# Optimization experiments

Measured on AMD Instinct MI355X. Metric: run time of the kernel, lower is better.

The kernel has to match this reference:

```python
import jax, jax.numpy as jnp
import numpy as np

IN_DIM = 512
OUT_DIM = 512
GRID_SIZE = 7
K = 4
N_KNOTS = GRID_SIZE + 2 * K + 1  # 16
N_BASIS = GRID_SIZE + K          # 11
BATCH = 16384


def b_splines(x, grid, k):
    # x: (B, in_dim), grid: (in_dim, N_KNOTS)
    x = x[..., None]  # (B, in, 1)
    value = ((x >= grid[:, :-1]) & (x < grid[:, 1:])).astype(x.dtype)  # (B, in, N_KNOTS-1)
    for p in range(1, k + 1):
        diff_left = grid[:, p:-1] - grid[:, :-(p + 1)]
        diff_right = grid[:, p + 1:] - grid[:, 1:-p]
        safe_dl = jnp.where(diff_left != 0, diff_left, 1.0)
        safe_dr = jnp.where(diff_right != 0, diff_right, 1.0)
        ratio_left = jnp.where(diff_left != 0, (x - grid[:, :-(p + 1)]) / safe_dl, 0.0)
        ratio_right = jnp.where(diff_right != 0, (grid[:, p + 1:] - x) / safe_dr, 0.0)
        value = (ratio_left * value[..., :-1] + ratio_right * value[..., 1:]) / (
            ratio_left + ratio_right + 1e-8)
    return value  # (B, in, N_BASIS)


def setup_inputs() -> dict:
    key = jax.random.key(0)
    k1, k2, k3, k4 = jax.random.split(key, 4)
    x = jax.random.uniform(k1, (BATCH, IN_DIM), dtype=jnp.float32)
    grid = jnp.tile(jnp.linspace(-1.0, 1.0, N_KNOTS, dtype=jnp.float32)[None, :], (IN_DIM, 1))
    coeff = jax.random.normal(k2, (OUT_DIM, IN_DIM, N_BASIS), dtype=jnp.float32) * 0.05
    scale_base = 1.0 / IN_DIM ** 0.5 + (
        jax.random.normal(k3, (OUT_DIM, IN_DIM), dtype=jnp.float32) * 2.0 - 1.0) * 0.05
    scale_spline = jnp.ones((OUT_DIM, IN_DIM), dtype=jnp.float32)
    bias = jnp.zeros((1, OUT_DIM), dtype=jnp.float32)
    return {"x": x, "grid": grid, "coeff": coeff, "scale_base": scale_base,
            "scale_spline": scale_spline, "bias": bias}


def reference(x, grid, coeff, scale_base, scale_spline, bias):
    shape = x.shape[:-1]
    x2 = x.reshape(-1, IN_DIM)
    splines = b_splines(x2, grid, K)                         # (B, in, N_BASIS)
    base_act = x2 + jnp.sin(x2)                              # KolmogorovActivation
    y_b = jnp.einsum('bi,oi->bo', base_act, scale_base)
    y_spline = jnp.einsum('bik,oik->bo', splines, coeff * scale_spline[:, :, None])
    y = y_b + y_spline + bias
    return y.reshape(*shape, OUT_DIM)
```

## Files before the change

kernel.cpp:

```cpp
#include <hip/hip_runtime.h>
#include <hip/hip_bf16.h>
#include <stdint.h>

#define IN_DIM  512
#define OUT_DIM 512
#define BATCH   16384
#define BM      128
#define BN      256
#define BK      96
#define KCH     64
#define TSTR    104
#define TILE_U  3072
#define TILE_EL 24576

typedef __bf16 bf16;
typedef __bf16 bf16x8 __attribute__((ext_vector_type(8)));
typedef float  f32x4  __attribute__((ext_vector_type(4)));

__device__ __forceinline__ uint bfbits(float v) {
    union { bf16 h; ushort u; } c; c.h = (bf16)v; return (uint)c.u;
}
__device__ __forceinline__ uint pk2(float lo, float hi) {
    return bfbits(lo) | (bfbits(hi) << 16);
}

__global__ void pack_w(const float* __restrict__ coeff,
                       const float* __restrict__ sbase,
                       const float* __restrict__ sspl,
                       bf16* __restrict__ W3) {
    __shared__ __align__(16) bf16 L[256 * 96];
    const int t  = threadIdx.x;
    const int g  = blockIdx.x >> 6;
    const int kc = blockIdx.x & 63;
    const int o  = g * 256 + t;
    const float* cp = coeff + ((size_t)o * 512 + kc * 8) * 11;
    const float* sp = sspl  + (size_t)o * 512 + kc * 8;
    const float* bp = sbase + (size_t)o * 512 + kc * 8;
    union { bf16 h[96]; uint4 q[12]; } rw;
#pragma unroll
    for (int il = 0; il < 8; ++il) {
        const float s = sp[il];
#pragma unroll
        for (int k = 0; k < 11; ++k) rw.h[il * 12 + k] = (bf16)(cp[il * 11 + k] * s);
        rw.h[il * 12 + 11] = (bf16)bp[il];
    }
    uint4* lrow = (uint4*)(L + t * 96);
#pragma unroll
    for (int j = 0; j < 12; ++j) lrow[j] = rw.q[j];
    __syncthreads();
    uint4* dst = (uint4*)W3 + (size_t)(g * 64 + kc) * TILE_U;
#pragma unroll
    for (int uu = 0; uu < 12; ++uu) {
        const int U   = uu * 256 + t;
        const int rb  = U / 192;
        const int rem = U - rb * 192;
        const int s   = rem >> 6;
        const int li  = rem & 63;
        const int lq  = li >> 4, lr = li & 15;
        dst[U] = *(const uint4*)(L + (rb * 16 + lr) * 96 + s * 32 + lq * 8);
    }
}


#define LOAD_B(Barr, kcn)                                                     \
  {                                                                           \
    const bf16* _bb = WgB + (size_t)(kcn) * TILE_EL + boff;                   \
    _Pragma("unroll")                                                         \
    for (int f = 0; f < 12; ++f)                                              \
      Barr[f] = *(const bf16x8*)(_bb + (f / 3) * 1536 + (f % 3) * 512);       \
  }

#define EVALP(kcn, Adst)                                                      \
  {                                                                           \
    float2 _xc = xn;                                                          \
    xn = *(const float2*)(xrow + ((((kcn) + 1) & 63) << 3));                  \
    evalPair(_xc, (Adst));                                                    \
  }

#define MFMA_PH(Ap, Barr)                                                     \
  {                                                                           \
    _Pragma("unroll")                                                         \
    for (int s = 0; s < 3; ++s) {                                             \
      bf16x8 af[4];                                                           \
      _Pragma("unroll")                                                       \
      for (int mt = 0; mt < 4; ++mt)                                          \
        af[mt] = *(const bf16x8*)&(Ap)[(wm * 64 + mt * 16 + lr) * TSTR + s * 32 + lq * 8]; \
      __builtin_amdgcn_s_setprio(1);                                          \
      _Pragma("unroll")                                                       \
      for (int mt = 0; mt < 4; ++mt)                                          \
        _Pragma("unroll")                                                     \
        for (int nt = 0; nt < 4; ++nt)                                        \
          acc[mt][nt] = __builtin_amdgcn_mfma_f32_16x16x32_bf16(              \
              af[mt], Barr[nt * 3 + s], acc[mt][nt], 0, 0, 0);                \
      __builtin_amdgcn_s_setprio(0);                                          \
    }                                                                         \
  }

__global__ void __launch_bounds__(512, 2) kan_gemm(
    const float* __restrict__ xg,
    const float* __restrict__ gridp,
    const float* __restrict__ bias,
    const bf16*  __restrict__ W3,
    float* __restrict__ out)
{
    __shared__ bf16 Abuf[2 * BM * TSTR];

    const int tid  = threadIdx.x;
    const int lane = tid & 63;
    const int wave = tid >> 6;
    const int bid = blockIdx.x;
    const int g   = (bid >> 2) & 1;
    const int mt_ = (bid >> 3) * 4 + (bid & 3);
    const int n0 = g * BN;
    const int m0 = mt_ * BM;

    const float g0    = gridp[0];
    const float inv_h = 1.0f / (gridp[1] - gridp[0]);

    const bf16* WgB = W3 + (size_t)g * KCH * TILE_EL;

    const int row_e = tid & 127;
    const int fpair = tid >> 7;
    const float* xrow = xg + (size_t)(m0 + row_e) * IN_DIM + fpair * 2;

    const int wm = wave & 1, wn = wave >> 1;
    const int lr = lane & 15, lq = lane >> 4;
    const bool mfirst = (wave >= 4);
    const int boff = wn * 6144 + lane * 8;

    bf16* const Ab0 = Abuf;
    bf16* const Ab1 = Abuf + BM * TSTR;

    f32x4 acc[4][4];
#pragma unroll
    for (int mt = 0; mt < 4; ++mt)
#pragma unroll
        for (int nt = 0; nt < 4; ++nt) { f32x4 z = {0.f, 0.f, 0.f, 0.f}; acc[mt][nt] = z; }

    bf16x8 Bc[12];
    float2 xn;

    auto evalOne = [&](float xv, uint* De) {
        float f  = __builtin_fmaf(xv, inv_h, -g0 * inv_h);
        f = fminf(fmaxf(f, 7.0f), 14.9999f);
        float fj = floorf(f);
        int   j0 = (int)fj;
        float t  = f - fj;
        float t1 = t + 1.0f, t2 = t + 2.0f, t3 = t + 3.0f;
        float s1 = 1.0f - t, s2 = 2.0f - t, s3 = 3.0f - t, s4 = 4.0f - t;
        float a0 = 0.5f * t, a1 = 0.5f * s1;
        const float i3 = (1.0f / 3.0f);
        float b0 = t  * a0 * i3;
        float b1 = (t1 * a1 + s2 * a0) * i3;
        float b2 = s1 * a1 * i3;
        float c0 = t  * b0 * 0.25f;
        float c1 = (t1 * b1 + s3 * b0) * 0.25f;
        float c2 = (t2 * b2 + s2 * b1) * 0.25f;
        float c3 = s1 * b2 * 0.25f;
        float w0 = t  * c0 * 0.2f;
        float w1 = (t1 * c1 + s4 * c0) * 0.2f;
        float w2 = (t2 * c2 + s3 * c1) * 0.2f;
        float w3 = (t3 * c3 + s2 * c2) * 0.2f;
        float w4 = s1 * c3 * 0.2f;
        const int q0 = j0 - 4;
        const int rr = q0 & 1;
        const int d  = q0 >> 1;
        uint P0 = pk2(w4, w3), P1 = pk2(w2, w1), P2 = bfbits(w0);
        uint A0 = rr ? (P0 << 16)                : P0;
        uint A1 = rr ? ((P0 >> 16) | (P1 << 16)) : P1;
        uint A2 = rr ? ((P1 >> 16) | (P2 << 16)) : P2;
        De[0] = 0u;
        De[1] = (d == 1) ? A0 : 0u;
        De[2] = (d == 2) ? A0 : ((d == 1) ? A1 : 0u);
        De[3] = (d == 3) ? A0 : ((d == 2) ? A1 : ((d == 1) ? A2 : 0u));
        De[4] = (d == 4) ? A0 : ((d == 3) ? A1 : ((d == 2) ? A2 : 0u));
        uint D5 = (d == 5) ? A0 : ((d == 4) ? A1 : ((d == 3) ? A2 : 0u));
        De[5] = (D5 & 0xFFFFu) | (bfbits(xv + __sinf(xv)) << 16);
    };
    auto evalPair = [&](float2 xc, bf16* Adst) {
        uint D[12];
        evalOne(xc.x, D);
        evalOne(xc.y, D + 6);
        uint4* awr = (uint4*)(Adst + row_e * TSTR + fpair * 24);
        awr[0] = make_uint4(D[0], D[1], D[2],  D[3]);
        awr[1] = make_uint4(D[4], D[5], D[6],  D[7]);
        awr[2] = make_uint4(D[8], D[9], D[10], D[11]);
    };

    LOAD_B(Bc, 0);
    {
        float2 xc0 = *(const float2*)(xrow);
        xn = *(const float2*)(xrow + 8);
        evalPair(xc0, Ab0);
    }
    __syncthreads();

    for (int kc = 0; kc < KCH; ++kc) {
        const int p = kc & 1;
        const bf16* Ap = p ? Ab1 : Ab0;
        bf16*       An = p ? Ab0 : Ab1;
        if (mfirst) {
            MFMA_PH(Ap, Bc);
            if (kc < KCH - 1) {
                LOAD_B(Bc, kc + 1);
                EVALP(kc + 1, An);
            }
        } else {
            if (kc < KCH - 1) EVALP(kc + 1, An);
            MFMA_PH(Ap, Bc);
            if (kc < KCH - 1) LOAD_B(Bc, kc + 1);
        }
        __syncthreads();
    }

#pragma unroll
    for (int nt = 0; nt < 4; ++nt) {
        const int gcol = n0 + wn * 64 + nt * 16 + lr;
        const float bv = bias[gcol];
#pragma unroll
        for (int mt = 0; mt < 4; ++mt) {
#pragma unroll
            for (int i = 0; i < 4; ++i) {
                const int grow = m0 + wm * 64 + mt * 16 + lq * 4 + i;
                out[(size_t)grow * OUT_DIM + gcol] = acc[mt][nt][i] + bv;
            }
        }
    }
}

extern "C" void kernel_launch(void* const* d_in, const int* in_sizes, int n_in,
                              void* d_out, int out_size, void* d_ws, size_t ws_size,
                              hipStream_t stream) {
    const float* x     = (const float*)d_in[0];
    const float* gridv = (const float*)d_in[1];
    const float* coeff = (const float*)d_in[2];
    const float* sbase = (const float*)d_in[3];
    const float* sspl  = (const float*)d_in[4];
    const float* bias  = (const float*)d_in[5];
    float* out = (float*)d_out;
    bf16*  W3  = (bf16*)d_ws;

    pack_w<<<dim3(128), 256, 0, stream>>>(coeff, sbase, sspl, W3);
    kan_gemm<<<dim3(256), 512, 0, stream>>>(x, gridv, bias, W3, out);
}
```

Baseline: 195.0 us.

## Halve M tile to 64 rows and double grid to 512 blocks

Shrinks the block's batch tile from 128 to 64 rows, so each thread now evaluates one spline feature instead of a pair and each wave computes a 32x64 output sub-tile. The grid doubles to 512 blocks, which gives more parallelism across the GPU's compute units and halves the per-thread accumulator registers. In exchange, each B (weight) tile loaded from global memory is reused across half as many rows, so weight traffic doubles and MFMA work per synchronization step drops.

```diff
diff --git a/kernel.cpp b/kernel.cpp
--- a/kernel.cpp
+++ b/kernel.cpp
@@ -5,7 +5,7 @@
 #define IN_DIM  512
 #define OUT_DIM 512
 #define BATCH   16384
-#define BM      128
+#define BM      64
 #define BN      256
 #define BK      96
 #define KCH     64
@@ -72,22 +72,22 @@
 
 #define EVALP(kcn, Adst)                                                      \
   {                                                                           \
-    float2 _xc = xn;                                                          \
-    xn = *(const float2*)(xrow + ((((kcn) + 1) & 63) << 3));                  \
-    evalPair(_xc, (Adst));                                                    \
+    float _xc = xn;                                                           \
+    xn = xrow[(((kcn) + 1) & 63) << 3];                                       \
+    evalF(_xc, (Adst));                                                       \
   }
 
 #define MFMA_PH(Ap, Barr)                                                     \
   {                                                                           \
     _Pragma("unroll")                                                         \
     for (int s = 0; s < 3; ++s) {                                             \
-      bf16x8 af[4];                                                           \
+      bf16x8 af[2];                                                           \
       _Pragma("unroll")                                                       \
-      for (int mt = 0; mt < 4; ++mt)                                          \
-        af[mt] = *(const bf16x8*)&(Ap)[(wm * 64 + mt * 16 + lr) * TSTR + s * 32 + lq * 8]; \
+      for (int mt = 0; mt < 2; ++mt)                                          \
+        af[mt] = *(const bf16x8*)&(Ap)[(wm * 32 + mt * 16 + lr) * TSTR + s * 32 + lq * 8]; \
       __builtin_amdgcn_s_setprio(1);                                          \
       _Pragma("unroll")                                                       \
-      for (int mt = 0; mt < 4; ++mt)                                          \
+      for (int mt = 0; mt < 2; ++mt)                                          \
         _Pragma("unroll")                                                     \
         for (int nt = 0; nt < 4; ++nt)                                        \
           acc[mt][nt] = __builtin_amdgcn_mfma_f32_16x16x32_bf16(              \
@@ -119,9 +119,9 @@
 
     const bf16* WgB = W3 + (size_t)g * KCH * TILE_EL;
 
-    const int row_e = tid & 127;
-    const int fpair = tid >> 7;
-    const float* xrow = xg + (size_t)(m0 + row_e) * IN_DIM + fpair * 2;
+    const int row_e = tid & 63;
+    const int fe    = tid >> 6;
+    const float* xrow = xg + (size_t)(m0 + row_e) * IN_DIM + fe;
 
     const int wm = wave & 1, wn = wave >> 1;
     const int lr = lane & 15, lq = lane >> 4;
@@ -131,14 +131,14 @@
     bf16* const Ab0 = Abuf;
     bf16* const Ab1 = Abuf + BM * TSTR;
 
-    f32x4 acc[4][4];
-#pragma unroll
-    for (int mt = 0; mt < 4; ++mt)
+    f32x4 acc[2][4];
+#pragma unroll
+    for (int mt = 0; mt < 2; ++mt)
 #pragma unroll
         for (int nt = 0; nt < 4; ++nt) { f32x4 z = {0.f, 0.f, 0.f, 0.f}; acc[mt][nt] = z; }
 
     bf16x8 Bc[12];
-    float2 xn;
+    float xn;
 
     auto evalOne = [&](float xv, uint* De) {
         float f  = __builtin_fmaf(xv, inv_h, -g0 * inv_h);
@@ -177,21 +177,20 @@
         uint D5 = (d == 5) ? A0 : ((d == 4) ? A1 : ((d == 3) ? A2 : 0u));
         De[5] = (D5 & 0xFFFFu) | (bfbits(xv + __sinf(xv)) << 16);
     };
-    auto evalPair = [&](float2 xc, bf16* Adst) {
-        uint D[12];
-        evalOne(xc.x, D);
-        evalOne(xc.y, D + 6);
-        uint4* awr = (uint4*)(Adst + row_e * TSTR + fpair * 24);
-        awr[0] = make_uint4(D[0], D[1], D[2],  D[3]);
-        awr[1] = make_uint4(D[4], D[5], D[6],  D[7]);
-        awr[2] = make_uint4(D[8], D[9], D[10], D[11]);
+    auto evalF = [&](float xc, bf16* Adst) {
+        uint D[6];
+        evalOne(xc, D);
+        uint2* awr = (uint2*)(Adst + row_e * TSTR + fe * 12);
+        awr[0] = make_uint2(D[0], D[1]);
+        awr[1] = make_uint2(D[2], D[3]);
+        awr[2] = make_uint2(D[4], D[5]);
     };
 
     LOAD_B(Bc, 0);
     {
-        float2 xc0 = *(const float2*)(xrow);
-        xn = *(const float2*)(xrow + 8);
-        evalPair(xc0, Ab0);
+        float xc0 = xrow[0];
+        xn = xrow[8];
+        evalF(xc0, Ab0);
     }
     __syncthreads();
 
@@ -218,10 +217,10 @@
         const int gcol = n0 + wn * 64 + nt * 16 + lr;
         const float bv = bias[gcol];
 #pragma unroll
-        for (int mt = 0; mt < 4; ++mt) {
+        for (int mt = 0; mt < 2; ++mt) {
 #pragma unroll
             for (int i = 0; i < 4; ++i) {
-                const int grow = m0 + wm * 64 + mt * 16 + lq * 4 + i;
+                const int grow = m0 + wm * 32 + mt * 16 + lq * 4 + i;
                 out[(size_t)grow * OUT_DIM + gcol] = acc[mt][nt][i] + bv;
             }
         }
@@ -241,5 +240,5 @@
     bf16*  W3  = (bf16*)d_ws;
 
     pack_w<<<dim3(128), 256, 0, stream>>>(coeff, sbase, sspl, W3);
-    kan_gemm<<<dim3(256), 512, 0, stream>>>(x, gridv, bias, W3, out);
-}
+    kan_gemm<<<dim3(512), 512, 0, stream>>>(x, gridv, bias, W3, out);
+}
```

Result: slower. 261.8 us (+34.3%).

## Process two K-chunks per barrier with double-pair LDS buffering

Applied to the files above, without the earlier changes.

The A-tile LDS buffer grows to four slots, and the main loop now handles two K-chunks per iteration, so there is one __syncthreads per pair of chunks instead of one per chunk. Spline evaluation and B prefetch for each chunk are interleaved between the two MFMA phases. This halves the number of block barriers but doubles LDS use, which may limit occupancy at 2 blocks per CU. It also adds register pressure from the extra x prefetch registers.

```diff
diff --git a/kernel.cpp b/kernel.cpp
--- a/kernel.cpp
+++ b/kernel.cpp
@@ -68,13 +68,6 @@
     _Pragma("unroll")                                                         \
     for (int f = 0; f < 12; ++f)                                              \
       Barr[f] = *(const bf16x8*)(_bb + (f / 3) * 1536 + (f % 3) * 512);       \
-  }
-
-#define EVALP(kcn, Adst)                                                      \
-  {                                                                           \
-    float2 _xc = xn;                                                          \
-    xn = *(const float2*)(xrow + ((((kcn) + 1) & 63) << 3));                  \
-    evalPair(_xc, (Adst));                                                    \
   }
 
 #define MFMA_PH(Ap, Barr)                                                     \
@@ -103,7 +96,7 @@
     const bf16*  __restrict__ W3,
     float* __restrict__ out)
 {
-    __shared__ bf16 Abuf[2 * BM * TSTR];
+    __shared__ bf16 Abuf[2 * 2 * BM * TSTR];
 
     const int tid  = threadIdx.x;
     const int lane = tid & 63;
@@ -128,9 +121,6 @@
     const bool mfirst = (wave >= 4);
     const int boff = wn * 6144 + lane * 8;
 
-    bf16* const Ab0 = Abuf;
-    bf16* const Ab1 = Abuf + BM * TSTR;
-
     f32x4 acc[4][4];
 #pragma unroll
     for (int mt = 0; mt < 4; ++mt)
@@ -138,7 +128,7 @@
         for (int nt = 0; nt < 4; ++nt) { f32x4 z = {0.f, 0.f, 0.f, 0.f}; acc[mt][nt] = z; }
 
     bf16x8 Bc[12];
-    float2 xn;
+    float2 xnA, xnB;
 
     auto evalOne = [&](float xv, uint* De) {
         float f  = __builtin_fmaf(xv, inv_h, -g0 * inv_h);
@@ -190,25 +180,53 @@
     LOAD_B(Bc, 0);
     {
         float2 xc0 = *(const float2*)(xrow);
-        xn = *(const float2*)(xrow + 8);
-        evalPair(xc0, Ab0);
+        float2 xc1 = *(const float2*)(xrow + 8);
+        xnA = *(const float2*)(xrow + 16);
+        xnB = *(const float2*)(xrow + 24);
+        evalPair(xc0, Abuf);
+        evalPair(xc1, Abuf + BM * TSTR);
     }
     __syncthreads();
 
-    for (int kc = 0; kc < KCH; ++kc) {
-        const int p = kc & 1;
-        const bf16* Ap = p ? Ab1 : Ab0;
-        bf16*       An = p ? Ab0 : Ab1;
+    for (int ph = 0; ph < 32; ++ph) {
+        const int pb = ph & 1;
+        const bf16* Ap0 = Abuf + (pb * 2 + 0) * BM * TSTR;
+        const bf16* Ap1 = Abuf + (pb * 2 + 1) * BM * TSTR;
+        bf16* An0 = Abuf + ((pb ^ 1) * 2 + 0) * BM * TSTR;
+        bf16* An1 = Abuf + ((pb ^ 1) * 2 + 1) * BM * TSTR;
+        const int kc0 = 2 * ph;
+        const bool more = (ph < 31);
+
         if (mfirst) {
-            MFMA_PH(Ap, Bc);
-            if (kc < KCH - 1) {
-                LOAD_B(Bc, kc + 1);
-                EVALP(kc + 1, An);
+            MFMA_PH(Ap0, Bc);
+            LOAD_B(Bc, kc0 + 1);
+            if (more) {
+                float2 xc = xnA;
+                xnA = *(const float2*)(xrow + (((kc0 + 4) & 63) << 3));
+                evalPair(xc, An0);
+            }
+            MFMA_PH(Ap1, Bc);
+            if (more) {
+                LOAD_B(Bc, kc0 + 2);
+                float2 xc = xnB;
+                xnB = *(const float2*)(xrow + (((kc0 + 5) & 63) << 3));
+                evalPair(xc, An1);
             }
         } else {
-            if (kc < KCH - 1) EVALP(kc + 1, An);
-            MFMA_PH(Ap, Bc);
-            if (kc < KCH - 1) LOAD_B(Bc, kc + 1);
+            if (more) {
+                float2 xc = xnA;
+                xnA = *(const float2*)(xrow + (((kc0 + 4) & 63) << 3));
+                evalPair(xc, An0);
+            }
+            MFMA_PH(Ap0, Bc);
+            LOAD_B(Bc, kc0 + 1);
+            if (more) {
+                float2 xc = xnB;
+                xnB = *(const float2*)(xrow + (((kc0 + 5) & 63) << 3));
+                evalPair(xc, An1);
+            }
+            MFMA_PH(Ap1, Bc);
+            if (more) LOAD_B(Bc, kc0 + 2);
         }
         __syncthreads();
     }
```

Measured after the change: 193.5 us. Within noise of the previous version (-0.8%).

## Switch GEMM to 32x32x16 bf16 MFMA with matching weight packing layout

Applied to the files above, without the earlier changes.

Replaces the 16x16x32 MFMA tiling (4x4 tiles per wave) with 32x32x16 MFMA (2x2 tiles per wave). The packed weight layout, the B-fragment loads, the A-fragment LDS reads and the output row mapping all change to fit the new instruction shape. The aim is fewer MFMA issues and fewer LDS A-fragment reads per k-chunk, since each larger instruction does more work per operand fetch. The cost is longer-latency instructions and a changed register and LDS access pattern, which may hurt overlap with the spline evaluation.

```diff
diff --git a/kernel.cpp b/kernel.cpp
--- a/kernel.cpp
+++ b/kernel.cpp
@@ -15,13 +15,14 @@
 
 typedef __bf16 bf16;
 typedef __bf16 bf16x8 __attribute__((ext_vector_type(8)));
-typedef float  f32x4  __attribute__((ext_vector_type(4)));
+typedef float  f32x16 __attribute__((ext_vector_type(16)));
 
 __device__ __forceinline__ uint bfbits(float v) {
     union { bf16 h; ushort u; } c; c.h = (bf16)v; return (uint)c.u;
 }
 __device__ __forceinline__ uint pk2(float lo, float hi) {
-    return bfbits(lo) | (bfbits(hi) << 16);
+    union { bf16 h; ushort u; } a, b; a.h = (bf16)lo; b.h = (bf16)hi;
+    return (uint)a.u | ((uint)b.u << 16);
 }
 
 __global__ void pack_w(const float* __restrict__ coeff,
@@ -52,12 +53,13 @@
 #pragma unroll
     for (int uu = 0; uu < 12; ++uu) {
         const int U   = uu * 256 + t;
-        const int rb  = U / 192;
-        const int rem = U - rb * 192;
-        const int s   = rem >> 6;
+        const int nb  = U / 384;
+        const int rem = U - nb * 384;
+        const int ks  = rem >> 6;
         const int li  = rem & 63;
-        const int lq  = li >> 4, lr = li & 15;
-        dst[U] = *(const uint4*)(L + (rb * 16 + lr) * 96 + s * 32 + lq * 8);
+        const int col = nb * 32 + (li & 31);
+        const int kk  = ks * 16 + (li >> 5) * 8;
+        dst[U] = *(const uint4*)(L + col * 96 + kk);
     }
 }
 
@@ -67,7 +69,7 @@
     const bf16* _bb = WgB + (size_t)(kcn) * TILE_EL + boff;                   \
     _Pragma("unroll")                                                         \
     for (int f = 0; f < 12; ++f)                                              \
-      Barr[f] = *(const bf16x8*)(_bb + (f / 3) * 1536 + (f % 3) * 512);       \
+      Barr[f] = *(const bf16x8*)(_bb + f * 512);                              \
   }
 
 #define EVALP(kcn, Adst)                                                      \
@@ -80,18 +82,18 @@
 #define MFMA_PH(Ap, Barr)                                                     \
   {                                                                           \
     _Pragma("unroll")                                                         \
-    for (int s = 0; s < 3; ++s) {                                             \
-      bf16x8 af[4];                                                           \
+    for (int ks = 0; ks < 6; ++ks) {                                          \
+      bf16x8 af[2];                                                           \
       _Pragma("unroll")                                                       \
-      for (int mt = 0; mt < 4; ++mt)                                          \
-        af[mt] = *(const bf16x8*)&(Ap)[(wm * 64 + mt * 16 + lr) * TSTR + s * 32 + lq * 8]; \
+      for (int mi = 0; mi < 2; ++mi)                                          \
+        af[mi] = *(const bf16x8*)&(Ap)[(wm * 64 + mi * 32 + l31) * TSTR + ks * 16 + hi * 8]; \
       __builtin_amdgcn_s_setprio(1);                                          \
       _Pragma("unroll")                                                       \
-      for (int mt = 0; mt < 4; ++mt)                                          \
+      for (int mi = 0; mi < 2; ++mi)                                          \
         _Pragma("unroll")                                                     \
-        for (int nt = 0; nt < 4; ++nt)                                        \
-          acc[mt][nt] = __builtin_amdgcn_mfma_f32_16x16x32_bf16(              \
-              af[mt], Barr[nt * 3 + s], acc[mt][nt], 0, 0, 0);                \
+        for (int ni = 0; ni < 2; ++ni)                                        \
+          acc[mi][ni] = __builtin_amdgcn_mfma_f32_32x32x16_bf16(              \
+              af[mi], Barr[ni * 6 + ks], acc[mi][ni], 0, 0, 0);               \
       __builtin_amdgcn_s_setprio(0);                                          \
     }                                                                         \
   }
@@ -124,18 +126,20 @@
     const float* xrow = xg + (size_t)(m0 + row_e) * IN_DIM + fpair * 2;
 
     const int wm = wave & 1, wn = wave >> 1;
-    const int lr = lane & 15, lq = lane >> 4;
+    const int l31 = lane & 31, hi = lane >> 5;
     const bool mfirst = (wave >= 4);
     const int boff = wn * 6144 + lane * 8;
 
     bf16* const Ab0 = Abuf;
     bf16* const Ab1 = Abuf + BM * TSTR;
 
-    f32x4 acc[4][4];
-#pragma unroll
-    for (int mt = 0; mt < 4; ++mt)
-#pragma unroll
-        for (int nt = 0; nt < 4; ++nt) { f32x4 z = {0.f, 0.f, 0.f, 0.f}; acc[mt][nt] = z; }
+    f32x16 acc[2][2];
+#pragma unroll
+    for (int mi = 0; mi < 2; ++mi)
+#pragma unroll
+        for (int ni = 0; ni < 2; ++ni)
+#pragma unroll
+            for (int r = 0; r < 16; ++r) acc[mi][ni][r] = 0.f;
 
     bf16x8 Bc[12];
     float2 xn;
@@ -214,15 +218,15 @@
     }
 
 #pragma unroll
-    for (int nt = 0; nt < 4; ++nt) {
-        const int gcol = n0 + wn * 64 + nt * 16 + lr;
+    for (int ni = 0; ni < 2; ++ni) {
+        const int gcol = n0 + wn * 64 + ni * 32 + l31;
         const float bv = bias[gcol];
 #pragma unroll
-        for (int mt = 0; mt < 4; ++mt) {
-#pragma unroll
-            for (int i = 0; i < 4; ++i) {
-                const int grow = m0 + wm * 64 + mt * 16 + lq * 4 + i;
-                out[(size_t)grow * OUT_DIM + gcol] = acc[mt][nt][i] + bv;
+        for (int mi = 0; mi < 2; ++mi) {
+#pragma unroll
+            for (int r = 0; r < 16; ++r) {
+                const int grow = m0 + wm * 64 + mi * 32 + (r & 3) + 8 * (r >> 2) + 4 * hi;
+                out[(size_t)grow * OUT_DIM + gcol] = acc[mi][ni][r] + bv;
             }
         }
     }
```

Result: slower. 199.7 us (+2.4%).
